# Kernel tuning notes

Measured on AMD Instinct MI355X. Metric: run time of the kernel, lower is better.

The kernel has to match this reference:

```python
import jax, jax.numpy as jnp
import numpy as np

N_NODES = 50000
N_EDGES = 800000
D_FEAT = 96
HIDDEN = 256
OUT = 40


def setup_inputs() -> dict:
    key = jax.random.key(0)
    ks = jax.random.split(key, 10)
    features = jax.random.normal(ks[0], (N_NODES, D_FEAT), dtype=jnp.float32)
    src = jax.random.randint(ks[1], (N_EDGES,), 0, N_NODES, dtype=jnp.int32)
    dst = jax.random.randint(ks[2], (N_EDGES,), 0, N_NODES, dtype=jnp.int32)
    def lin(k, fan_in, fan_out):
        bound = 1.0 / np.sqrt(fan_in)
        kw, kb = jax.random.split(k)
        W = jax.random.uniform(kw, (fan_in, fan_out), jnp.float32, -bound, bound)
        b = jax.random.uniform(kb, (fan_out,), jnp.float32, -bound, bound)
        return W, b
    W1, b1 = lin(ks[3], 2 * D_FEAT, HIDDEN)
    W2, b2 = lin(ks[4], HIDDEN, HIDDEN)
    W3, b3 = lin(ks[5], HIDDEN, OUT)
    return {"features": features, "src": src, "dst": dst,
            "W1": W1, "b1": b1, "W2": W2, "b2": b2, "W3": W3, "b3": b3}


def reference(features, src, dst, W1, b1, W2, b2, W3, b3):
    # neighbor mean: gather src features, segment-sum into dst, divide by degree
    gathered = features[src]                                  # [E, D]
    summed = jax.ops.segment_sum(gathered, dst, num_segments=N_NODES)  # [N, D]
    deg = jax.ops.segment_sum(jnp.ones((N_EDGES,), jnp.float32), dst,
                              num_segments=N_NODES)           # [N]
    neighbor_feats = summed / jnp.maximum(deg, 1.0)[:, None]  # zero where no neighbors
    combined = jnp.concatenate([features, neighbor_feats], axis=1)  # [N, 2D]
    x = jax.nn.relu(combined @ W1 + b1)
    x = jax.nn.relu(x @ W2 + b2)
    return x @ W3 + b3
```

## Files before the change

### kernel.cpp

```cpp
#include <hip/hip_runtime.h>

#define N_NODES 50000
#define N_EDGES 800000
#define DF      96
#define HID     256
#define OUTF    40
#define BM      64
#define NPART   512
#define CS      32
#define PCAP2   2048

#define EPB     2048
#define NBE     ((N_EDGES + EPB - 1) / EPB)

#define FEAT_THREADS (N_NODES * DF / 8)
#define FEAT_BLKS ((FEAT_THREADS + 255) / 256)
#define WSHUF_ELEMS ((96 + 128 + 24) * 512)
#define WSHUF_BLKS (WSHUF_ELEMS / 256)

typedef __attribute__((ext_vector_type(8))) short bf16x8;
typedef __attribute__((ext_vector_type(4))) float f32x4;

static __device__ __forceinline__ unsigned short f2bf(float f) {
    unsigned int u = __float_as_uint(f);
    u += 0x7fffu + ((u >> 16) & 1u);
    return (unsigned short)(u >> 16);
}
static __device__ __forceinline__ int part_of(int d) {
    return (int)(((long long)d * NPART) / N_NODES);
}
static __device__ __forceinline__ int part_n0(int p) {
    return (int)(((long long)p * N_NODES + NPART - 1) / NPART);
}

__global__ __launch_bounds__(256) void k1_prep_bin(
    const float* __restrict__ feat, const float* __restrict__ W1,
    const float* __restrict__ W2, const float* __restrict__ W3,
    const int* __restrict__ src, const int* __restrict__ dst,
    uint4* __restrict__ featbf, unsigned short* __restrict__ W1s,
    unsigned short* __restrict__ W2s, unsigned short* __restrict__ W3s,
    unsigned int* __restrict__ packed2, int* __restrict__ cellCnt)
{
    const int bid = blockIdx.x, t = threadIdx.x;
    if (bid < FEAT_BLKS) {
        int i = bid * 256 + t;
        if (i < FEAT_THREADS) {
            const float4* p = reinterpret_cast<const float4*>(feat) + (size_t)i * 2;
            float4 v0 = p[0], v1 = p[1];
            uint4 pk;
            pk.x = (unsigned)f2bf(v0.x) | ((unsigned)f2bf(v0.y) << 16);
            pk.y = (unsigned)f2bf(v0.z) | ((unsigned)f2bf(v0.w) << 16);
            pk.z = (unsigned)f2bf(v1.x) | ((unsigned)f2bf(v1.y) << 16);
            pk.w = (unsigned)f2bf(v1.z) | ((unsigned)f2bf(v1.w) << 16);
            featbf[i] = pk;
        }
        return;
    }
    if (bid < FEAT_BLKS + WSHUF_BLKS) {
        int i = (bid - FEAT_BLKS) * 256 + t;
        int j  = i & 7;
        int l  = (i >> 3) & 63;
        int fi = i >> 9;
        int kg = l >> 4, n16 = l & 15;
        if (fi < 96) {
            int tt = fi / 6, s = fi % 6;
            int k = s * 32 + kg * 8 + j, n = tt * 16 + n16;
            W1s[i] = f2bf(W1[(size_t)k * HID + n]);
        } else if (fi < 96 + 128) {
            int f2 = fi - 96;
            int tt = f2 / 8, s = f2 % 8;
            int k = s * 32 + kg * 8 + j, n = tt * 16 + n16;
            W2s[i - 96 * 512] = f2bf(W2[(size_t)k * HID + n]);
        } else {
            int f3 = fi - 224;
            int tt = f3 / 8, s = f3 % 8;
            int k = s * 32 + kg * 8 + j, n = tt * 16 + n16;
            W3s[i - 224 * 512] = (n < OUTF) ? f2bf(W3[(size_t)k * OUTF + n])
                                            : (unsigned short)0;
        }
        return;
    }
    {
        __shared__ int cur[NPART];
        const int bid2 = bid - FEAT_BLKS - WSHUF_BLKS;
        cur[t] = 0;
        cur[t + 256] = 0;
        __syncthreads();
        int pv[8], pos[8];
        unsigned pkv[8];
        bool valid[8];
#pragma unroll
        for (int k = 0; k < 8; ++k) {
            int e = bid2 * EPB + k * 256 + t;
            valid[k] = (e < N_EDGES);
            pv[k] = 0; pkv[k] = 0; pos[k] = CS;
            if (valid[k]) {
                int d = dst[e], s = src[e];
                int p = part_of(d);
                pv[k] = p;
                pkv[k] = ((unsigned)(d - part_n0(p)) << 16) | (unsigned)s;
                pos[k] = atomicAdd(&cur[p], 1);
            }
        }
        __syncthreads();
#pragma unroll
        for (int q = 0; q < 2; ++q) {
            int pp = q * 256 + t;
            cellCnt[(size_t)pp * NBE + bid2] = (cur[pp] < CS) ? cur[pp] : CS;
        }
#pragma unroll
        for (int k = 0; k < 8; ++k) {
            if (valid[k] && pos[k] < CS)
                packed2[((size_t)pv[k] * NBE + bid2) * CS + pos[k]] = pkv[k];
        }
    }
}

__global__ __launch_bounds__(1024, 4) void part_agg(
    const unsigned int* __restrict__ packed2, const int* __restrict__ cellCnt,
    const unsigned int* __restrict__ featbf, unsigned int* __restrict__ nbr32)
{
    __shared__ int hist[128];
    __shared__ int scanex[128];
    __shared__ int cur[128];
    __shared__ int nodeOff[128];
    __shared__ int nodeCnt[128];
    __shared__ unsigned short srcLDS[PCAP2];
    const int p = blockIdx.x, t = threadIdx.x;
    const int n0 = part_n0(p);
    const int nl = part_n0(p + 1) - n0;
    const unsigned int* cells = packed2 + (size_t)p * NBE * CS;
    const int* ccnt = cellCnt + (size_t)p * NBE;

    if (t < 128) hist[t] = 0;
    __syncthreads();
    for (int c = t; c < NBE; c += 1024) {
        int cnt = ccnt[c];
        const unsigned int* cp = cells + (size_t)c * CS;
        for (int i = 0; i < cnt; ++i)
            atomicAdd(&hist[cp[i] >> 16], 1);
    }
    __syncthreads();
    int v = 0;
    if (t < 128) { v = hist[t]; scanex[t] = v; }
    __syncthreads();
    for (int off = 1; off < 128; off <<= 1) {
        int x = 0;
        if (t < 128 && t >= off) x = scanex[t - off];
        __syncthreads();
        if (t < 128) scanex[t] += x;
        __syncthreads();
    }
    if (t < 128) {
        int ex = scanex[t] - v;
        cur[t] = ex;
        nodeOff[t] = ex;
        nodeCnt[t] = v;
    }
    __syncthreads();
    for (int c = t; c < NBE; c += 1024) {
        int cnt = ccnt[c];
        const unsigned int* cp = cells + (size_t)c * CS;
        for (int i = 0; i < cnt; ++i) {
            unsigned pk = cp[i];
            int r = atomicAdd(&cur[pk >> 16], 1);
            if (r < PCAP2) srcLDS[r] = (unsigned short)(pk & 0xffffu);
        }
    }
    __syncthreads();
    const int wv = t >> 6, lane = t & 63;
    const bool act = (lane < 48);
    for (int n = wv; n < nl; n += 16) {
        int beg = nodeOff[n];
        int cnt = nodeCnt[n];
        float a0 = 0.f, a1 = 0.f;
        int j = 0;
        for (; j + 8 <= cnt; j += 8) {
            unsigned u[8];
            if (act) {
#pragma unroll
                for (int q = 0; q < 8; ++q)
                    u[q] = featbf[(size_t)srcLDS[beg + j + q] * 48 + lane];
#pragma unroll
                for (int q = 0; q < 8; ++q) {
                    a0 += __uint_as_float(u[q] << 16);
                    a1 += __uint_as_float(u[q] & 0xffff0000u);
                }
            }
        }
        for (; j + 2 <= cnt; j += 2) {
            if (act) {
                unsigned u0 = featbf[(size_t)srcLDS[beg + j] * 48 + lane];
                unsigned u1 = featbf[(size_t)srcLDS[beg + j + 1] * 48 + lane];
                a0 += __uint_as_float(u0 << 16) + __uint_as_float(u1 << 16);
                a1 += __uint_as_float(u0 & 0xffff0000u)
                    + __uint_as_float(u1 & 0xffff0000u);
            }
        }
        if (j < cnt && act) {
            unsigned u0 = featbf[(size_t)srcLDS[beg + j] * 48 + lane];
            a0 += __uint_as_float(u0 << 16);
            a1 += __uint_as_float(u0 & 0xffff0000u);
        }
        float inv = 1.0f / fmaxf((float)cnt, 1.0f);
        if (act)
            nbr32[(size_t)(n0 + n) * 48 + lane] =
                (unsigned)f2bf(a0 * inv) | ((unsigned)f2bf(a1 * inv) << 16);
    }
}

__global__ __launch_bounds__(512, 4) void mlp3(
    const unsigned int* __restrict__ featbf, const unsigned int* __restrict__ nbr32,
    const unsigned short* __restrict__ W1s, const float* __restrict__ b1,
    const unsigned short* __restrict__ W2s, const float* __restrict__ b2,
    const unsigned short* __restrict__ W3s, const float* __restrict__ b3,
    float* __restrict__ out)
{
    __shared__ __align__(16) char bufA[BM * 512];
    __shared__ __align__(16) char bufB[BM * 512];

    const int t = threadIdx.x;
    const int lane = t & 63;
    const int w = t >> 6;
    const int row0 = blockIdx.x * BM;
    const int n16 = lane & 15;
    const int kg = lane >> 4;

    for (int i = t; i < BM * 24; i += 512) {
        int row = i / 24, c = i % 24;
        int half = (c >= 12) ? 1 : 0;
        int cg = c - half * 12;
        int grow = row0 + row;
        int lds_byte = (row * 384 + half * 192 + cg * 16) ^ ((row & 7) << 4);
        uint4 v = make_uint4(0u, 0u, 0u, 0u);
        if (grow < N_NODES) {
            const unsigned int* s = half ? nbr32 : featbf;
            v = *reinterpret_cast<const uint4*>(s + (size_t)grow * 48 + cg * 4);
        }
        *reinterpret_cast<uint4*>(bufA + lds_byte) = v;
    }
    __syncthreads();

    {
        f32x4 acc[4][2];
#pragma unroll
        for (int tt = 0; tt < 2; ++tt) {
            float bb = b1[(w * 2 + tt) * 16 + n16];
#pragma unroll
            for (int mt = 0; mt < 4; ++mt) {
                acc[mt][tt][0] = bb; acc[mt][tt][1] = bb;
                acc[mt][tt][2] = bb; acc[mt][tt][3] = bb;
            }
        }
#pragma unroll
        for (int s = 0; s < 6; ++s) {
            bf16x8 a[4], b[2];
#pragma unroll
            for (int mt = 0; mt < 4; ++mt) {
                int m = mt * 16 + n16;
                int byte_ = (m * 384 + s * 64 + kg * 16) ^ ((m & 7) << 4);
                a[mt] = *reinterpret_cast<const bf16x8*>(bufA + byte_);
            }
#pragma unroll
            for (int tt = 0; tt < 2; ++tt)
                b[tt] = *reinterpret_cast<const bf16x8*>(
                    W1s + ((size_t)((w * 2 + tt) * 6 + s) * 64 + lane) * 8);
#pragma unroll
            for (int mt = 0; mt < 4; ++mt)
#pragma unroll
                for (int tt = 0; tt < 2; ++tt)
                    acc[mt][tt] = __builtin_amdgcn_mfma_f32_16x16x32_bf16(
                        a[mt], b[tt], acc[mt][tt], 0, 0, 0);
        }
#pragma unroll
        for (int mt = 0; mt < 4; ++mt)
#pragma unroll
            for (int tt = 0; tt < 2; ++tt) {
                int col = (w * 2 + tt) * 16 + n16;
#pragma unroll
                for (int r = 0; r < 4; ++r) {
                    int row = mt * 16 + kg * 4 + r;
                    int byte_ = (row * 512 + col * 2) ^ ((row & 7) << 4);
                    *reinterpret_cast<unsigned short*>(bufB + byte_) =
                        f2bf(fmaxf(acc[mt][tt][r], 0.f));
                }
            }
    }
    __syncthreads();

    {
        f32x4 acc[4][2];
#pragma unroll
        for (int tt = 0; tt < 2; ++tt) {
            float bb = b2[(w * 2 + tt) * 16 + n16];
#pragma unroll
            for (int mt = 0; mt < 4; ++mt) {
                acc[mt][tt][0] = bb; acc[mt][tt][1] = bb;
                acc[mt][tt][2] = bb; acc[mt][tt][3] = bb;
            }
        }
#pragma unroll
        for (int s = 0; s < 8; ++s) {
            bf16x8 a[4], b[2];
#pragma unroll
            for (int mt = 0; mt < 4; ++mt) {
                int m = mt * 16 + n16;
                int byte_ = (m * 512 + s * 64 + kg * 16) ^ ((m & 7) << 4);
                a[mt] = *reinterpret_cast<const bf16x8*>(bufB + byte_);
            }
#pragma unroll
            for (int tt = 0; tt < 2; ++tt)
                b[tt] = *reinterpret_cast<const bf16x8*>(
                    W2s + ((size_t)((w * 2 + tt) * 8 + s) * 64 + lane) * 8);
#pragma unroll
            for (int mt = 0; mt < 4; ++mt)
#pragma unroll
                for (int tt = 0; tt < 2; ++tt)
                    acc[mt][tt] = __builtin_amdgcn_mfma_f32_16x16x32_bf16(
                        a[mt], b[tt], acc[mt][tt], 0, 0, 0);
        }
#pragma unroll
        for (int mt = 0; mt < 4; ++mt)
#pragma unroll
            for (int tt = 0; tt < 2; ++tt) {
                int col = (w * 2 + tt) * 16 + n16;
#pragma unroll
                for (int r = 0; r < 4; ++r) {
                    int row = mt * 16 + kg * 4 + r;
                    int byte_ = (row * 512 + col * 2) ^ ((row & 7) << 4);
                    *reinterpret_cast<unsigned short*>(bufA + byte_) =
                        f2bf(fmaxf(acc[mt][tt][r], 0.f));
                }
            }
    }
    __syncthreads();

    {
        const int mt3 = w & 3;
        const int tb  = (w >> 2) ? 2 : 0;
        const int nt3 = (w >> 2) ? 1 : 2;
        f32x4 acc3[2];
#pragma unroll
        for (int tt = 0; tt < 2; ++tt) {
            int col = (tb + tt) * 16 + n16;
            float bb = (tt < nt3 && col < OUTF) ? b3[col] : 0.f;
            acc3[tt][0] = bb; acc3[tt][1] = bb; acc3[tt][2] = bb; acc3[tt][3] = bb;
        }
#pragma unroll
        for (int s = 0; s < 8; ++s) {
            int m = mt3 * 16 + n16;
            int byte_ = (m * 512 + s * 64 + kg * 16) ^ ((m & 7) << 4);
            bf16x8 a = *reinterpret_cast<const bf16x8*>(bufA + byte_);
#pragma unroll
            for (int tt = 0; tt < 2; ++tt) {
                if (tt < nt3) {
                    bf16x8 b = *reinterpret_cast<const bf16x8*>(
                        W3s + ((size_t)((tb + tt) * 8 + s) * 64 + lane) * 8);
                    acc3[tt] = __builtin_amdgcn_mfma_f32_16x16x32_bf16(
                        a, b, acc3[tt], 0, 0, 0);
                }
            }
        }
#pragma unroll
        for (int tt = 0; tt < 2; ++tt) {
            int col = (tb + tt) * 16 + n16;
            if (tt < nt3 && col < OUTF) {
#pragma unroll
                for (int r = 0; r < 4; ++r) {
                    int row = row0 + mt3 * 16 + kg * 4 + r;
                    if (row < N_NODES)
                        out[(size_t)row * OUTF + col] = acc3[tt][r];
                }
            }
        }
    }
}

extern "C" void kernel_launch(void* const* d_in, const int* in_sizes, int n_in,
                              void* d_out, int out_size, void* d_ws, size_t ws_size,
                              hipStream_t stream)
{
    const float* feat = (const float*)d_in[0];
    const int*   src  = (const int*)d_in[1];
    const int*   dst  = (const int*)d_in[2];
    const float* W1   = (const float*)d_in[3];
    const float* b1   = (const float*)d_in[4];
    const float* W2   = (const float*)d_in[5];
    const float* b2   = (const float*)d_in[6];
    const float* W3   = (const float*)d_in[7];
    const float* b3   = (const float*)d_in[8];
    float* out = (float*)d_out;

    int* cellCnt = (int*)d_ws;
    unsigned int* packed2 = (unsigned int*)(cellCnt + (size_t)NPART * NBE);
    unsigned int* featbf = packed2 + (size_t)NPART * NBE * CS;
    unsigned int* nbr32  = featbf + (size_t)N_NODES * 48;
    unsigned short* W1s  = (unsigned short*)(nbr32 + (size_t)N_NODES * 48);
    unsigned short* W2s  = W1s + 96 * 512;
    unsigned short* W3s  = W2s + 128 * 512;

    k1_prep_bin<<<FEAT_BLKS + WSHUF_BLKS + NBE, 256, 0, stream>>>(
        feat, W1, W2, W3, src, dst,
        (uint4*)featbf, W1s, W2s, W3s, packed2, cellCnt);

    part_agg<<<NPART, 1024, 0, stream>>>(packed2, cellCnt, featbf, nbr32);

    mlp3<<<(N_NODES + BM - 1) / BM, 512, 0, stream>>>(
        featbf, nbr32, W1s, b1, W2s, b2, W3s, b3, out);
}
```

Baseline: 79.01 us.

## Fuse neighbor aggregation into MLP kernel with 64-node partitions

Partitions are now aligned to the 64-row MLP tile (dst>>6), so each MLP block builds its own CSR from the binned edge cells, gathers and averages neighbor features straight into shared memory, then runs the three-layer MLP. This drops the separate aggregation kernel and the global round trip of the neighbor-feature buffer. The cell size shrinks to 20 and per-partition source capacity to 1536, which raises the risk of silently dropping edges on overflow. Each MLP block also now does serialized histogram and scatter work before its matmuls, and more shared memory per block may lower occupancy.

After: 89.90 us. 1.14x slower.

```diff
diff --git a/kernel.cpp b/kernel.cpp
--- a/kernel.cpp
+++ b/kernel.cpp
@@ -6,9 +6,9 @@
 #define HID     256
 #define OUTF    40
 #define BM      64
-#define NPART   512
-#define CS      32
-#define PCAP2   2048
+#define NPART   782
+#define CS      20
+#define SCAP    1536
 
 #define EPB     2048
 #define NBE     ((N_EDGES + EPB - 1) / EPB)
@@ -25,12 +25,6 @@
     unsigned int u = __float_as_uint(f);
     u += 0x7fffu + ((u >> 16) & 1u);
     return (unsigned short)(u >> 16);
-}
-static __device__ __forceinline__ int part_of(int d) {
-    return (int)(((long long)d * NPART) / N_NODES);
-}
-static __device__ __forceinline__ int part_n0(int p) {
-    return (int)(((long long)p * N_NODES + NPART - 1) / NPART);
 }
 
 __global__ __launch_bounds__(256) void k1_prep_bin(
@@ -83,8 +77,7 @@
     {
         __shared__ int cur[NPART];
         const int bid2 = bid - FEAT_BLKS - WSHUF_BLKS;
-        cur[t] = 0;
-        cur[t + 256] = 0;
+        for (int i = t; i < NPART; i += 256) cur[i] = 0;
         __syncthreads();
         int pv[8], pos[8];
         unsigned pkv[8];
@@ -96,18 +89,15 @@
             pv[k] = 0; pkv[k] = 0; pos[k] = CS;
             if (valid[k]) {
                 int d = dst[e], s = src[e];
-                int p = part_of(d);
+                int p = d >> 6;
                 pv[k] = p;
-                pkv[k] = ((unsigned)(d - part_n0(p)) << 16) | (unsigned)s;
+                pkv[k] = ((unsigned)(d & 63) << 16) | (unsigned)s;
                 pos[k] = atomicAdd(&cur[p], 1);
             }
         }
         __syncthreads();
-#pragma unroll
-        for (int q = 0; q < 2; ++q) {
-            int pp = q * 256 + t;
-            cellCnt[(size_t)pp * NBE + bid2] = (cur[pp] < CS) ? cur[pp] : CS;
-        }
+        for (int i = t; i < NPART; i += 256)
+            cellCnt[(size_t)i * NBE + bid2] = (cur[i] < CS) ? cur[i] : CS;
 #pragma unroll
         for (int k = 0; k < 8; ++k) {
             if (valid[k] && pos[k] < CS)
@@ -116,101 +106,9 @@
     }
 }
 
-__global__ __launch_bounds__(1024, 4) void part_agg(
+__global__ __launch_bounds__(512, 4) void part_mlp(
     const unsigned int* __restrict__ packed2, const int* __restrict__ cellCnt,
-    const unsigned int* __restrict__ featbf, unsigned int* __restrict__ nbr32)
-{
-    __shared__ int hist[128];
-    __shared__ int scanex[128];
-    __shared__ int cur[128];
-    __shared__ int nodeOff[128];
-    __shared__ int nodeCnt[128];
-    __shared__ unsigned short srcLDS[PCAP2];
-    const int p = blockIdx.x, t = threadIdx.x;
-    const int n0 = part_n0(p);
-    const int nl = part_n0(p + 1) - n0;
-    const unsigned int* cells = packed2 + (size_t)p * NBE * CS;
-    const int* ccnt = cellCnt + (size_t)p * NBE;
-
-    if (t < 128) hist[t] = 0;
-    __syncthreads();
-    for (int c = t; c < NBE; c += 1024) {
-        int cnt = ccnt[c];
-        const unsigned int* cp = cells + (size_t)c * CS;
-        for (int i = 0; i < cnt; ++i)
-            atomicAdd(&hist[cp[i] >> 16], 1);
-    }
-    __syncthreads();
-    int v = 0;
-    if (t < 128) { v = hist[t]; scanex[t] = v; }
-    __syncthreads();
-    for (int off = 1; off < 128; off <<= 1) {
-        int x = 0;
-        if (t < 128 && t >= off) x = scanex[t - off];
-        __syncthreads();
-        if (t < 128) scanex[t] += x;
-        __syncthreads();
-    }
-    if (t < 128) {
-        int ex = scanex[t] - v;
-        cur[t] = ex;
-        nodeOff[t] = ex;
-        nodeCnt[t] = v;
-    }
-    __syncthreads();
-    for (int c = t; c < NBE; c += 1024) {
-        int cnt = ccnt[c];
-        const unsigned int* cp = cells + (size_t)c * CS;
-        for (int i = 0; i < cnt; ++i) {
-            unsigned pk = cp[i];
-            int r = atomicAdd(&cur[pk >> 16], 1);
-            if (r < PCAP2) srcLDS[r] = (unsigned short)(pk & 0xffffu);
-        }
-    }
-    __syncthreads();
-    const int wv = t >> 6, lane = t & 63;
-    const bool act = (lane < 48);
-    for (int n = wv; n < nl; n += 16) {
-        int beg = nodeOff[n];
-        int cnt = nodeCnt[n];
-        float a0 = 0.f, a1 = 0.f;
-        int j = 0;
-        for (; j + 8 <= cnt; j += 8) {
-            unsigned u[8];
-            if (act) {
-#pragma unroll
-                for (int q = 0; q < 8; ++q)
-                    u[q] = featbf[(size_t)srcLDS[beg + j + q] * 48 + lane];
-#pragma unroll
-                for (int q = 0; q < 8; ++q) {
-                    a0 += __uint_as_float(u[q] << 16);
-                    a1 += __uint_as_float(u[q] & 0xffff0000u);
-                }
-            }
-        }
-        for (; j + 2 <= cnt; j += 2) {
-            if (act) {
-                unsigned u0 = featbf[(size_t)srcLDS[beg + j] * 48 + lane];
-                unsigned u1 = featbf[(size_t)srcLDS[beg + j + 1] * 48 + lane];
-                a0 += __uint_as_float(u0 << 16) + __uint_as_float(u1 << 16);
-                a1 += __uint_as_float(u0 & 0xffff0000u)
-                    + __uint_as_float(u1 & 0xffff0000u);
-            }
-        }
-        if (j < cnt && act) {
-            unsigned u0 = featbf[(size_t)srcLDS[beg + j] * 48 + lane];
-            a0 += __uint_as_float(u0 << 16);
-            a1 += __uint_as_float(u0 & 0xffff0000u);
-        }
-        float inv = 1.0f / fmaxf((float)cnt, 1.0f);
-        if (act)
-            nbr32[(size_t)(n0 + n) * 48 + lane] =
-                (unsigned)f2bf(a0 * inv) | ((unsigned)f2bf(a1 * inv) << 16);
-    }
-}
-
-__global__ __launch_bounds__(512, 4) void mlp3(
-    const unsigned int* __restrict__ featbf, const unsigned int* __restrict__ nbr32,
+    const unsigned int* __restrict__ featbf,
     const unsigned short* __restrict__ W1s, const float* __restrict__ b1,
     const unsigned short* __restrict__ W2s, const float* __restrict__ b2,
     const unsigned short* __restrict__ W3s, const float* __restrict__ b3,
@@ -218,26 +116,112 @@
 {
     __shared__ __align__(16) char bufA[BM * 512];
     __shared__ __align__(16) char bufB[BM * 512];
-
-    const int t = threadIdx.x;
+    __shared__ int hist[64];
+    __shared__ int nodeOff[64];
+    __shared__ int nodeCnt[64];
+    __shared__ int curL[64];
+    __shared__ unsigned short srcLDS[SCAP];
+
+    const int p = blockIdx.x, t = threadIdx.x;
     const int lane = t & 63;
     const int w = t >> 6;
-    const int row0 = blockIdx.x * BM;
+    const int row0 = p * BM;
+    const unsigned int* cells = packed2 + (size_t)p * NBE * CS;
+    const int* ccnt = cellCnt + (size_t)p * NBE;
     const int n16 = lane & 15;
     const int kg = lane >> 4;
 
-    for (int i = t; i < BM * 24; i += 512) {
-        int row = i / 24, c = i % 24;
-        int half = (c >= 12) ? 1 : 0;
-        int cg = c - half * 12;
+    for (int i = t; i < BM * 12; i += 512) {
+        int row = i / 12, c4 = i % 12;
         int grow = row0 + row;
-        int lds_byte = (row * 384 + half * 192 + cg * 16) ^ ((row & 7) << 4);
+        int lds_byte = (row * 384 + c4 * 16) ^ ((row & 7) << 4);
         uint4 v = make_uint4(0u, 0u, 0u, 0u);
-        if (grow < N_NODES) {
-            const unsigned int* s = half ? nbr32 : featbf;
-            v = *reinterpret_cast<const uint4*>(s + (size_t)grow * 48 + cg * 4);
-        }
+        if (grow < N_NODES)
+            v = *reinterpret_cast<const uint4*>(featbf + (size_t)grow * 48 + c4 * 4);
         *reinterpret_cast<uint4*>(bufA + lds_byte) = v;
+    }
+
+    if (t < 64) hist[t] = 0;
+    __syncthreads();
+    for (int c = t; c < NBE; c += 512) {
+        int cnt = ccnt[c];
+        const unsigned int* cp = cells + (size_t)c * CS;
+        for (int i = 0; i < cnt; ++i)
+            atomicAdd(&hist[cp[i] >> 16], 1);
+    }
+    __syncthreads();
+    int v = 0;
+    if (t < 64) { v = hist[t]; nodeOff[t] = v; }
+    __syncthreads();
+    for (int off = 1; off < 64; off <<= 1) {
+        int x = 0;
+        if (t < 64 && t >= off) x = nodeOff[t - off];
+        __syncthreads();
+        if (t < 64) nodeOff[t] += x;
+        __syncthreads();
+    }
+    if (t < 64) {
+        int ex = nodeOff[t] - v;
+        nodeOff[t] = ex;
+        curL[t] = ex;
+        nodeCnt[t] = v;
+    }
+    __syncthreads();
+    for (int c = t; c < NBE; c += 512) {
+        int cnt = ccnt[c];
+        const unsigned int* cp = cells + (size_t)c * CS;
+        for (int i = 0; i < cnt; ++i) {
+            unsigned pk = cp[i];
+            int r = atomicAdd(&curL[pk >> 16], 1);
+            if (r < SCAP) srcLDS[r] = (unsigned short)(pk & 0xffffu);
+        }
+    }
+    __syncthreads();
+
+    {
+        const bool act = (lane < 48);
+#pragma unroll
+        for (int i = 0; i < 8; ++i) {
+            int n = w * 8 + i;
+            int grow = row0 + n;
+            int beg = 0, cnt = 0;
+            if (grow < N_NODES) { beg = nodeOff[n]; cnt = nodeCnt[n]; }
+            float a0 = 0.f, a1 = 0.f;
+            int j = 0;
+            for (; j + 8 <= cnt; j += 8) {
+                unsigned u[8];
+                if (act) {
+#pragma unroll
+                    for (int q = 0; q < 8; ++q)
+                        u[q] = featbf[(size_t)srcLDS[beg + j + q] * 48 + lane];
+#pragma unroll
+                    for (int q = 0; q < 8; ++q) {
+                        a0 += __uint_as_float(u[q] << 16);
+                        a1 += __uint_as_float(u[q] & 0xffff0000u);
+                    }
+                }
+            }
+            for (; j + 2 <= cnt; j += 2) {
+                if (act) {
+                    unsigned u0 = featbf[(size_t)srcLDS[beg + j] * 48 + lane];
+                    unsigned u1 = featbf[(size_t)srcLDS[beg + j + 1] * 48 + lane];
+                    a0 += __uint_as_float(u0 << 16) + __uint_as_float(u1 << 16);
+                    a1 += __uint_as_float(u0 & 0xffff0000u)
+                        + __uint_as_float(u1 & 0xffff0000u);
+                }
+            }
+            if (j < cnt && act) {
+                unsigned u0 = featbf[(size_t)srcLDS[beg + j] * 48 + lane];
+                a0 += __uint_as_float(u0 << 16);
+                a1 += __uint_as_float(u0 & 0xffff0000u);
+            }
+            float inv = 1.0f / fmaxf((float)cnt, 1.0f);
+            unsigned pk = (unsigned)f2bf(a0 * inv) | ((unsigned)f2bf(a1 * inv) << 16);
+            if (act) {
+                int byte_ = (n * 384 + 192 + lane * 4) ^ ((n & 7) << 4);
+                *reinterpret_cast<unsigned int*>(bufA + byte_) = pk;
+            }
+        }
     }
     __syncthreads();
 
@@ -394,8 +378,7 @@
     int* cellCnt = (int*)d_ws;
     unsigned int* packed2 = (unsigned int*)(cellCnt + (size_t)NPART * NBE);
     unsigned int* featbf = packed2 + (size_t)NPART * NBE * CS;
-    unsigned int* nbr32  = featbf + (size_t)N_NODES * 48;
-    unsigned short* W1s  = (unsigned short*)(nbr32 + (size_t)N_NODES * 48);
+    unsigned short* W1s  = (unsigned short*)(featbf + (size_t)N_NODES * 48);
     unsigned short* W2s  = W1s + 96 * 512;
     unsigned short* W3s  = W2s + 128 * 512;
 
@@ -403,8 +386,6 @@
         feat, W1, W2, W3, src, dst,
         (uint4*)featbf, W1s, W2s, W3s, packed2, cellCnt);
 
-    part_agg<<<NPART, 1024, 0, stream>>>(packed2, cellCnt, featbf, nbr32);
-
-    mlp3<<<(N_NODES + BM - 1) / BM, 512, 0, stream>>>(
-        featbf, nbr32, W1s, b1, W2s, b2, W3s, b3, out);
+    part_mlp<<<NPART, 512, 0, stream>>>(
+        packed2, cellCnt, featbf, W1s, b1, W2s, b2, W3s, b3, out);
 }
```
